# Performance work log

Hardware: AMD Instinct MI355X
Metric: run time of the kernel (lower is better)

## Reference

```python
import jax, jax.numpy as jnp
import numpy as np

K = 16  # kNN neighbors
R = 4   # upsampling ratio


def knn_idx(x, k):
    """Per-cloud kNN (self excluded). x: [B,N,C] -> idx [B,N,k] int32."""
    sq = jnp.sum(x * x, axis=-1)  # [B,N]
    d = sq[:, :, None] + sq[:, None, :] - 2.0 * jnp.einsum('bnc,bmc->bnm', x, x)
    n = x.shape[1]
    d = d + jnp.eye(n, dtype=x.dtype) * jnp.asarray(1e9, x.dtype)  # exclude self-loop
    _, idx = jax.lax.top_k(-d, k)  # k smallest distances
    return idx


def edge_conv(x, idx, W, b):
    """EdgeConv: mlp([x_i, x_j - x_i]) with max aggregation over neighbors.
    x: [B,N,C], idx: [B,N,k] -> [B,N,out]."""
    nbr = jax.vmap(lambda xb, ib: xb[ib])(x, idx)            # [B,N,k,C] gather
    ctr = jnp.broadcast_to(x[:, :, None, :], nbr.shape)
    e = jnp.concatenate([ctr, nbr - ctr], axis=-1)           # [B,N,k,2C]
    h = jax.nn.relu(jnp.einsum('bnkc,cd->bnkd', e, W) + b)
    return jnp.max(h, axis=2)                                # max aggregate


def setup_inputs() -> dict:
    key = jax.random.key(0)
    ks = jax.random.split(key, 16)
    B, N = 8, 2048
    chans = [3, 32, 32, 64]  # DynConv stack: 3->32->32->64
    C = chans[-1]

    def lin(k, fan_in, fan_out):
        s = 1.0 / np.sqrt(fan_in)
        return jax.random.uniform(k, (fan_in, fan_out), jnp.float32, -s, s)

    inp = {'x': jax.random.normal(ks[0], (B, N, 3), jnp.float32)}
    # DynConv (EdgeConv) weights: Linear(2*in, out)
    for i in range(3):
        inp[f'W{i}'] = lin(ks[1 + i], 2 * chans[i], chans[i + 1])
        inp[f'b{i}'] = jnp.zeros((chans[i + 1],), jnp.float32)
    # NodeShuffle: EdgeConv(C -> R*C) then shuffle N -> N*R
    inp['Wup'] = lin(ks[5], 2 * C, R * C)
    inp['bup'] = jnp.zeros((R * C,), jnp.float32)
    # Reconstructor MLP([64,128,64,3])
    rdims = [64, 128, 64, 3]
    for i in range(3):
        inp[f'Wr{i}'] = lin(ks[6 + i], rdims[i], rdims[i + 1])
        inp[f'br{i}'] = jnp.zeros((rdims[i + 1],), jnp.float32)
    return inp


def reference(x, W0, b0, W1, b1, W2, b2, Wup, bup, Wr0, br0, Wr1, br1, Wr2, br2):
    # Dynamic feature extractor: recompute kNN on current feature space each layer
    for W, b in ((W0, b0), (W1, b1), (W2, b2)):
        idx = knn_idx(x, K)
        x = edge_conv(x, idx, W, b)
    # NodeShuffle upsampler: EdgeConv to R*C channels, then shuffle nodes
    idx = knn_idx(x, K)
    h = edge_conv(x, idx, Wup, bup)              # [B,N,R*C]
    B, N, _ = h.shape
    C = h.shape[-1] // R
    x = h.reshape(B, N, R, C).reshape(B, N * R, C)  # [B,N*R,C]
    # Reconstructor MLP -> xyz
    x = jax.nn.relu(x @ Wr0 + br0)
    x = jax.nn.relu(x @ Wr1 + br1)
    return x @ Wr2 + br2                          # [B,N*R,3]
```

## Files before the change

kernel.cpp:

```cpp
#include <hip/hip_runtime.h>

#define B_ 8
#define N_ 2048
#define K_ 16
#define M_ (B_*N_)

typedef unsigned long long ull;

__device__ __forceinline__ ull kmin(ull a, ull b) { return a < b ? a : b; }
__device__ __forceinline__ float  fmx(float a, float b)  { return fmaxf(a, b); }
__device__ __forceinline__ double fmx(double a, double b){ return fmax(a, b); }

__global__ __launch_bounds__(256) void transpose_kernel(const float* __restrict__ X,
                                                        float* __restrict__ XT, int C) {
    int t = blockIdx.x * 256 + threadIdx.x;
    if (t >= M_ * C) return;
    int c = t >> 14;
    int m = t & (M_ - 1);
    int b = m >> 11, n = m & (N_ - 1);
    XT[((size_t)b * C + c) * N_ + n] = X[(size_t)m * C + c];
}

template<int C>
__global__ __launch_bounds__(256, 2) void knnD_kernel(const float* __restrict__ XT,
                                                      int* __restrict__ idx_out) {
    constexpr int TJ = 128;
    constexpr int SJ = TJ + 4;
    constexpr int SS = TJ + 12;
    __shared__ float xiT[C][36];
    __shared__ float xjT[C][SJ];
    __shared__ float S[32][SS];

    int tid = threadIdx.x;
    int sb = (blockIdx.x & 7) * (M_ / 32 / 8) + (blockIdx.x >> 3);
    int m0 = sb * 32;
    int b  = m0 >> 11;
    int i0 = m0 & (N_ - 1);
    const float* XTb = XT + (size_t)b * C * N_;

    for (int e4 = tid; e4 < C * 8; e4 += 256) {
        int c = e4 >> 3, ch = e4 & 7;
        *(float4*)&xiT[c][ch * 4] = *(const float4*)&XTb[(size_t)c * N_ + i0 + ch * 4];
    }

    ull t[16];
#pragma unroll
    for (int q = 0; q < 16; ++q) t[q] = ~0ull;
    float t15f = __uint_as_float(0x7FFFFFFFu);

    int ig = tid >> 5, jl4 = tid & 31;
    int irow = tid >> 3, r = tid & 7;
    int i_loc = i0 + irow;

    for (int jt = 0; jt < N_ / TJ; ++jt) {
        __syncthreads();
        for (int e4 = tid; e4 < C * 32; e4 += 256) {
            int c = e4 >> 5, ch = e4 & 31;
            *(float4*)&xjT[c][ch * 4] =
                *(const float4*)&XTb[(size_t)c * N_ + jt * TJ + ch * 4];
        }
        __syncthreads();

        float acc[4][4];
#pragma unroll
        for (int u = 0; u < 4; ++u) {
            acc[u][0] = 0.f; acc[u][1] = 0.f; acc[u][2] = 0.f; acc[u][3] = 0.f;
        }
#pragma unroll 4
        for (int c = 0; c < C; ++c) {
            float4 xi4 = *(const float4*)&xiT[c][ig * 4];
            float4 xj4 = *(const float4*)&xjT[c][jl4 * 4];
            float xiv[4] = {xi4.x, xi4.y, xi4.z, xi4.w};
            float xjv[4] = {xj4.x, xj4.y, xj4.z, xj4.w};
#pragma unroll
            for (int u = 0; u < 4; ++u)
#pragma unroll
                for (int v = 0; v < 4; ++v) {
                    float df = xiv[u] - xjv[v];
                    acc[u][v] = fmaf(df, df, acc[u][v]);
                }
        }
#pragma unroll
        for (int u = 0; u < 4; ++u)
            *(float4*)&S[ig * 4 + u][jl4 * 4] =
                make_float4(acc[u][0], acc[u][1], acc[u][2], acc[u][3]);
        __syncthreads();

#pragma unroll
        for (int w = 0; w < 4; ++w) {
            float4 sv = *(const float4*)&S[irow][r * 4 + 32 * w];
            float se[4] = {sv.x, sv.y, sv.z, sv.w};
            float mn = fminf(fminf(se[0], se[1]), fminf(se[2], se[3]));
            if (!(mn > t15f)) {
                int jbase = jt * TJ + r * 4 + 32 * w;
#pragma unroll
                for (int e = 0; e < 4; ++e) {
                    float s = se[e];
                    if (!(s > t15f)) {
                        int jg = jbase + e;
                        if (jg != i_loc) {
                            unsigned uu = __float_as_uint(s) ^ 0x80000000u;
                            ull key = ((ull)uu << 32) | (unsigned)jg;
                            if (key < t[15]) {
                                t[15] = key;
#pragma unroll
                                for (int s2 = 15; s2 > 0; --s2) {
                                    ull a = t[s2 - 1], bb2 = t[s2];
                                    bool sw = bb2 < a;
                                    t[s2 - 1] = sw ? bb2 : a;
                                    t[s2]     = sw ? a : bb2;
                                }
                                t15f = __uint_as_float((unsigned)(t[15] >> 32) ^ 0x80000000u);
                            }
                        }
                    }
                }
            }
        }
    }

#pragma unroll
    for (int msk = 1; msk <= 4; msk <<= 1) {
        ull o[16];
#pragma unroll
        for (int q = 0; q < 16; ++q)
            o[q] = __shfl_xor((ull)t[q], msk, 64);
        ull nt[16];
#pragma unroll
        for (int q = 0; q < 16; ++q) nt[q] = kmin(t[q], o[15 - q]);
#pragma unroll
        for (int s2 = 8; s2 >= 1; s2 >>= 1) {
#pragma unroll
            for (int q = 0; q < 16; ++q) {
                if (!(q & s2)) {
                    ull a = nt[q], bb2 = nt[q | s2];
                    bool sw = bb2 < a;
                    nt[q]      = sw ? bb2 : a;
                    nt[q | s2] = sw ? a : bb2;
                }
            }
        }
#pragma unroll
        for (int q = 0; q < 16; ++q) t[q] = nt[q];
    }

    if (r == 0) {
        int* op = idx_out + (size_t)(m0 + irow) * K_;
#pragma unroll
        for (int q = 0; q < 16; ++q) op[q] = (int)(unsigned)(t[q] & 0xffffffffull);
    }
}

template<int C, typename TO>
__global__ __launch_bounds__(256) void proj_kernel(const float* __restrict__ X,
        const float* __restrict__ W, TO* __restrict__ T1NB,
        int Dfull, int DH, int doff) {
    __shared__ float XsT[C][68];
    __shared__ float Bs[C][64];
    int tid = threadIdx.x;
    int m0 = blockIdx.x * 64;
    int n0 = blockIdx.y * 64;

    if constexpr (C == 3) {
        if (tid < 192) { int row = tid / 3, c = tid - row * 3;
            XsT[c][row] = X[(size_t)(m0 + row) * 3 + c]; }
    } else {
        constexpr int C4 = C / 4;
        for (int e4 = tid; e4 < 64 * C4; e4 += 256) {
            int row = e4 / C4, c4 = e4 - row * C4;
            float4 v = *(const float4*)&X[(size_t)(m0 + row) * C + c4 * 4];
            XsT[c4*4+0][row] = v.x; XsT[c4*4+1][row] = v.y;
            XsT[c4*4+2][row] = v.z; XsT[c4*4+3][row] = v.w;
        }
    }
    for (int e = tid; e < C * 64; e += 256) {
        int c = e >> 6, dc = e & 63;
        int n = n0 + dc;
        float wv = (n < DH) ? W[(size_t)c * Dfull + doff + n]
                            : W[(size_t)(C + c) * Dfull + doff + (n - DH)];
        Bs[c][dc] = wv;
    }
    __syncthreads();

    int tx = tid & 15, ty = tid >> 4;
    double acc[4][4];
#pragma unroll
    for (int u = 0; u < 4; ++u) { acc[u][0]=0.0; acc[u][1]=0.0; acc[u][2]=0.0; acc[u][3]=0.0; }

#pragma unroll 4
    for (int c = 0; c < C; ++c) {
        float4 xv = *(const float4*)&XsT[c][ty * 4];
        float4 wv = *(const float4*)&Bs[c][tx * 4];
        double xd[4] = {(double)xv.x, (double)xv.y, (double)xv.z, (double)xv.w};
        double wd[4] = {(double)wv.x, (double)wv.y, (double)wv.z, (double)wv.w};
#pragma unroll
        for (int u = 0; u < 4; ++u)
#pragma unroll
            for (int v = 0; v < 4; ++v)
                acc[u][v] = fma(xd[u], wd[v], acc[u][v]);
    }
#pragma unroll
    for (int u = 0; u < 4; ++u) {
        TO* dst = &T1NB[(size_t)(m0 + ty * 4 + u) * (2 * DH) + n0 + tx * 4];
        if constexpr (sizeof(TO) == 8) {
            *(double2*)&dst[0] = make_double2(acc[u][0], acc[u][1]);
            *(double2*)&dst[2] = make_double2(acc[u][2], acc[u][3]);
        } else {
            *(float4*)&dst[0] = make_float4((float)acc[u][0], (float)acc[u][1],
                                            (float)acc[u][2], (float)acc[u][3]);
        }
    }
}

template<int DH, typename TE>
__global__ __launch_bounds__(256) void gmax_kernel(const TE* __restrict__ T1NB,
        const int* __restrict__ idx, const float* __restrict__ bias,
        float* __restrict__ O, int Dfull, int doff) {
    constexpr int TPP = DH / 2;
    constexpr int PPB = 256 / TPP;
    __shared__ int idxs[PPB * 16];

    int tid = threadIdx.x;
    int cpx = gridDim.x >> 3;
    int sb = ((int)blockIdx.x & 7) * cpx + ((int)blockIdx.x >> 3);
    int m0 = sb * PPB;

    if (tid < PPB * 16)
        idxs[tid] = idx[(size_t)(m0 + tid / 16) * K_ + (tid & 15)];
    __syncthreads();

    int p = tid / TPP, dh = tid % TPP;
    int d0 = dh * 2;
    int m = m0 + p;
    int b = m >> 11;
    size_t base = (size_t)m * (2 * DH);
    TE t1a = T1NB[base + d0],      t1b = T1NB[base + d0 + 1];
    TE nba = T1NB[base + DH + d0], nbb = T1NB[base + DH + d0 + 1];
    TE ba = t1a - nba, bb2 = t1b - nbb;
    TE ma = (TE)-1.0e30, mb = (TE)-1.0e30;
    size_t rowb = ((size_t)(b << 11)) * (2 * DH) + DH + d0;
    const int* ip = &idxs[p * 16];
#pragma unroll 4
    for (int k = 0; k < 16; ++k) {
        int j = ip[k];
        TE qa = T1NB[rowb + (size_t)j * (2 * DH)];
        TE qb = T1NB[rowb + (size_t)j * (2 * DH) + 1];
        ma = fmx(ma, ba + qa);
        mb = fmx(mb, bb2 + qb);
    }
    float2 o;
    o.x = (float)fmx(ma + (TE)bias[doff + d0],     (TE)0);
    o.y = (float)fmx(mb + (TE)bias[doff + d0 + 1], (TE)0);
    *(float2*)&O[(size_t)m * Dfull + doff + d0] = o;
}

__global__ __launch_bounds__(256) void recon_kernel(const float* __restrict__ U,
        const float* __restrict__ W0, const float* __restrict__ b0,
        const float* __restrict__ W1, const float* __restrict__ b1,
        const float* __restrict__ W2, const float* __restrict__ b2,
        float* __restrict__ O) {
    __shared__ float F[32 * 68];
    __shared__ float H1[128 * 33];
    __shared__ float H2[64 * 33];
    __shared__ float W2s[64 * 4];
    __shared__ float b0s[128], b1s[64], b2s[4];

    int tid = threadIdx.x;
    int m0 = blockIdx.x * 32;

    {
        const float4* src = (const float4*)(U + (size_t)m0 * 64);
        for (int e4 = tid; e4 < 32 * 16; e4 += 256) {
            int p = e4 >> 4, c4 = e4 & 15;
            *(float4*)&F[p * 68 + c4 * 4] = src[e4];
        }
    }
    if (tid < 192) W2s[(tid / 3) * 4 + (tid % 3)] = W2[tid];
    if (tid < 128) b0s[tid] = b0[tid];
    else if (tid < 192) b1s[tid - 128] = b1[tid - 128];
    else if (tid == 192) { b2s[0] = b2[0]; b2s[1] = b2[1]; b2s[2] = b2[2]; }
    __syncthreads();

    int p = tid >> 3, s = tid & 7;

    float acc[16];
#pragma unroll
    for (int q = 0; q < 16; ++q) acc[q] = 0.f;
    for (int c = 0; c < 64; ++c) {
        float a = F[p * 68 + c];
#pragma unroll
        for (int q = 0; q < 4; ++q) {
            float4 w = *(const float4*)&W0[c * 128 + s * 4 + q * 32];
            acc[q * 4 + 0] = fmaf(a, w.x, acc[q * 4 + 0]);
            acc[q * 4 + 1] = fmaf(a, w.y, acc[q * 4 + 1]);
            acc[q * 4 + 2] = fmaf(a, w.z, acc[q * 4 + 2]);
            acc[q * 4 + 3] = fmaf(a, w.w, acc[q * 4 + 3]);
        }
    }
#pragma unroll
    for (int q = 0; q < 4; ++q)
#pragma unroll
        for (int i2 = 0; i2 < 4; ++i2) {
            int dd = s * 4 + q * 32 + i2;
            H1[dd * 33 + p] = fmaxf(acc[q * 4 + i2] + b0s[dd], 0.f);
        }
    __syncthreads();

    float a2[8];
#pragma unroll
    for (int q = 0; q < 8; ++q) a2[q] = 0.f;
    for (int c = 0; c < 128; ++c) {
        float a = H1[c * 33 + p];
#pragma unroll
        for (int q = 0; q < 2; ++q) {
            float4 w = *(const float4*)&W1[c * 64 + s * 4 + q * 32];
            a2[q * 4 + 0] = fmaf(a, w.x, a2[q * 4 + 0]);
            a2[q * 4 + 1] = fmaf(a, w.y, a2[q * 4 + 1]);
            a2[q * 4 + 2] = fmaf(a, w.z, a2[q * 4 + 2]);
            a2[q * 4 + 3] = fmaf(a, w.w, a2[q * 4 + 3]);
        }
    }
#pragma unroll
    for (int q = 0; q < 2; ++q)
#pragma unroll
        for (int i2 = 0; i2 < 4; ++i2) {
            int dd = s * 4 + q * 32 + i2;
            H2[dd * 33 + p] = fmaxf(a2[q * 4 + i2] + b1s[dd], 0.f);
        }
    __syncthreads();

    if (tid < 96) {
        int p3 = tid / 3, d3 = tid - p3 * 3;
        float av = 0.f;
#pragma unroll
        for (int c = 0; c < 64; ++c)
            av = fmaf(H2[c * 33 + p3], W2s[c * 4 + d3], av);
        O[(size_t)(m0 + p3) * 3 + d3] = av + b2s[d3];
    }
}

extern "C" void kernel_launch(void* const* d_in, const int* in_sizes, int n_in,
                              void* d_out, int out_size, void* d_ws, size_t ws_size,
                              hipStream_t stream) {
    const float* x   = (const float*)d_in[0];
    const float* W0  = (const float*)d_in[1];
    const float* b0  = (const float*)d_in[2];
    const float* W1  = (const float*)d_in[3];
    const float* b1  = (const float*)d_in[4];
    const float* W2  = (const float*)d_in[5];
    const float* b2  = (const float*)d_in[6];
    const float* Wup = (const float*)d_in[7];
    const float* bup = (const float*)d_in[8];
    const float* Wr0 = (const float*)d_in[9];
    const float* br0 = (const float*)d_in[10];
    const float* Wr1 = (const float*)d_in[11];
    const float* br1 = (const float*)d_in[12];
    const float* Wr2 = (const float*)d_in[13];
    const float* br2 = (const float*)d_in[14];
    float* out = (float*)d_out;

    char* ws = (char*)d_ws;
    size_t o = 0;
    auto alloc = [&](size_t nbytes) {
        void* pp = ws + o;
        o += (nbytes + 255) & ~(size_t)255;
        return pp;
    };
    float*  X1    = (float*)alloc((size_t)M_ * 32 * 4);
    float*  X2    = (float*)alloc((size_t)M_ * 32 * 4);
    float*  X3    = (float*)alloc((size_t)M_ * 64 * 4);
    float*  H     = (float*)alloc((size_t)M_ * 256 * 4);
    int*    idxb  = (int*)alloc((size_t)M_ * 16 * 4);
    double* T1NBd = (double*)alloc((size_t)M_ * 128 * 8);
    float*  T1NBf = (float*)alloc((size_t)M_ * 256 * 4);
    float*  XT    = (float*)alloc((size_t)M_ * 64 * 4);

    transpose_kernel<<<(M_ * 3) / 256, 256, 0, stream>>>(x, XT, 3);
    knnD_kernel<3><<<512, 256, 0, stream>>>(XT, idxb);
    proj_kernel<3, double><<<dim3(M_ / 64, 1), 256, 0, stream>>>(x, W0, T1NBd, 32, 32, 0);
    gmax_kernel<32, double><<<M_ / 16, 256, 0, stream>>>(T1NBd, idxb, b0, X1, 32, 0);
    transpose_kernel<<<(M_ * 32) / 256, 256, 0, stream>>>(X1, XT, 32);
    knnD_kernel<32><<<512, 256, 0, stream>>>(XT, idxb);
    proj_kernel<32, double><<<dim3(M_ / 64, 1), 256, 0, stream>>>(X1, W1, T1NBd, 32, 32, 0);
    gmax_kernel<32, double><<<M_ / 16, 256, 0, stream>>>(T1NBd, idxb, b1, X2, 32, 0);
    transpose_kernel<<<(M_ * 32) / 256, 256, 0, stream>>>(X2, XT, 32);
    knnD_kernel<32><<<512, 256, 0, stream>>>(XT, idxb);
    proj_kernel<32, double><<<dim3(M_ / 64, 2), 256, 0, stream>>>(X2, W2, T1NBd, 64, 64, 0);
    gmax_kernel<64, double><<<M_ / 8, 256, 0, stream>>>(T1NBd, idxb, b2, X3, 64, 0);
    transpose_kernel<<<(M_ * 64) / 256, 256, 0, stream>>>(X3, XT, 64);
    knnD_kernel<64><<<512, 256, 0, stream>>>(XT, idxb);
    proj_kernel<64, float><<<dim3(M_ / 64, 4), 256, 0, stream>>>(X3, Wup, T1NBf, 256, 128, 0);
    gmax_kernel<128, float><<<M_ / 4, 256, 0, stream>>>(T1NBf, idxb, bup, H, 256, 0);
    proj_kernel<64, float><<<dim3(M_ / 64, 4), 256, 0, stream>>>(X3, Wup, T1NBf, 256, 128, 128);
    gmax_kernel<128, float><<<M_ / 4, 256, 0, stream>>>(T1NBf, idxb, bup, H, 256, 128);
    recon_kernel<<<2048, 256, 0, stream>>>(H, Wr0, br0, Wr1, br1, Wr2, br2, out);
}
```

Measured before the change: 1.150 ms.

## Pack kNN distance math into float2 vectors and chunk the j-tile over channels

The kNN distance kernel now computes squared differences with two-wide float vectors so the compiler can emit packed FP32 subtract and FMA instructions. The shared j-tile is staged in 32-channel chunks rather than holding all channels, which shrinks LDS use for C=64. The launch-bounds occupancy hint and the S row padding also change. Chunking adds extra barriers per tile, the new S padding may change bank conflicts, and the packed ops depend on the compiler actually emitting them.

```diff
diff --git a/kernel.cpp b/kernel.cpp
--- a/kernel.cpp
+++ b/kernel.cpp
@@ -6,6 +6,7 @@
 #define M_ (B_*N_)
 
 typedef unsigned long long ull;
+typedef float ev2 __attribute__((ext_vector_type(2)));
 
 __device__ __forceinline__ ull kmin(ull a, ull b) { return a < b ? a : b; }
 __device__ __forceinline__ float  fmx(float a, float b)  { return fmaxf(a, b); }
@@ -22,13 +23,14 @@
 }
 
 template<int C>
-__global__ __launch_bounds__(256, 2) void knnD_kernel(const float* __restrict__ XT,
-                                                      int* __restrict__ idx_out) {
-    constexpr int TJ = 128;
-    constexpr int SJ = TJ + 4;
-    constexpr int SS = TJ + 12;
+__global__ __launch_bounds__(256) void knnD_kernel(const float* __restrict__ XT,
+                                                   int* __restrict__ idx_out) {
+    constexpr int TJ  = 128;
+    constexpr int CH  = (C > 32) ? 32 : C;
+    constexpr int NCH = C / CH;
+    constexpr int SS  = TJ + 4;
     __shared__ float xiT[C][36];
-    __shared__ float xjT[C][SJ];
+    __shared__ float xjT[CH][TJ];
     __shared__ float S[32][SS];
 
     int tid = threadIdx.x;
@@ -53,37 +55,43 @@
     int i_loc = i0 + irow;
 
     for (int jt = 0; jt < N_ / TJ; ++jt) {
-        __syncthreads();
-        for (int e4 = tid; e4 < C * 32; e4 += 256) {
-            int c = e4 >> 5, ch = e4 & 31;
-            *(float4*)&xjT[c][ch * 4] =
-                *(const float4*)&XTb[(size_t)c * N_ + jt * TJ + ch * 4];
-        }
-        __syncthreads();
-
-        float acc[4][4];
+        ev2 acc2[4][2];
+#pragma unroll
+        for (int u = 0; u < 4; ++u) { acc2[u][0] = (ev2)0.f; acc2[u][1] = (ev2)0.f; }
+
+#pragma unroll
+        for (int ch = 0; ch < NCH; ++ch) {
+            int c0 = ch * CH;
+            __syncthreads();
+            for (int e4 = tid; e4 < CH * 32; e4 += 256) {
+                int cc = e4 >> 5, chh = e4 & 31;
+                *(float4*)&xjT[cc][chh * 4] =
+                    *(const float4*)&XTb[(size_t)(c0 + cc) * N_ + jt * TJ + chh * 4];
+            }
+            __syncthreads();
+
+#pragma unroll 4
+            for (int cc = 0; cc < CH; ++cc) {
+                float4 xi4 = *(const float4*)&xiT[c0 + cc][ig * 4];
+                float4 xj4 = *(const float4*)&xjT[cc][jl4 * 4];
+                ev2 xj01 = {xj4.x, xj4.y};
+                ev2 xj23 = {xj4.z, xj4.w};
+                float xiv[4] = {xi4.x, xi4.y, xi4.z, xi4.w};
+#pragma unroll
+                for (int u = 0; u < 4; ++u) {
+                    ev2 xiu = {xiv[u], xiv[u]};
+                    ev2 d0 = xj01 - xiu;
+                    ev2 d1 = xj23 - xiu;
+                    acc2[u][0] = __builtin_elementwise_fma(d0, d0, acc2[u][0]);
+                    acc2[u][1] = __builtin_elementwise_fma(d1, d1, acc2[u][1]);
+                }
+            }
+        }
 #pragma unroll
         for (int u = 0; u < 4; ++u) {
-            acc[u][0] = 0.f; acc[u][1] = 0.f; acc[u][2] = 0.f; acc[u][3] = 0.f;
-        }
-#pragma unroll 4
-        for (int c = 0; c < C; ++c) {
-            float4 xi4 = *(const float4*)&xiT[c][ig * 4];
-            float4 xj4 = *(const float4*)&xjT[c][jl4 * 4];
-            float xiv[4] = {xi4.x, xi4.y, xi4.z, xi4.w};
-            float xjv[4] = {xj4.x, xj4.y, xj4.z, xj4.w};
-#pragma unroll
-            for (int u = 0; u < 4; ++u)
-#pragma unroll
-                for (int v = 0; v < 4; ++v) {
-                    float df = xiv[u] - xjv[v];
-                    acc[u][v] = fmaf(df, df, acc[u][v]);
-                }
-        }
-#pragma unroll
-        for (int u = 0; u < 4; ++u)
-            *(float4*)&S[ig * 4 + u][jl4 * 4] =
-                make_float4(acc[u][0], acc[u][1], acc[u][2], acc[u][3]);
+            *(ev2*)&S[ig * 4 + u][jl4 * 4]     = acc2[u][0];
+            *(ev2*)&S[ig * 4 + u][jl4 * 4 + 2] = acc2[u][1];
+        }
         __syncthreads();
 
 #pragma unroll
```

Result: slower. 1.186 ms (+3.1%).
